# Kernel optimization log

Hardware: AMD Instinct MI355X
Metric: run time of the kernel (lower is better)

Reference implementation:

```python
import jax, jax.numpy as jnp
import numpy as np

EPS = 1e-8  # matches torch F.cosine_similarity eps default


def setup_inputs() -> dict:
    key = jax.random.key(0)
    k1, k2 = jax.random.split(key)
    z = jax.random.normal(k1, (8192, 256), dtype=jnp.float32)            # [N, d] node latents
    embedding_weight = jax.random.normal(k2, (4096, 256), dtype=jnp.float32)  # [V, d] codebook
    return {"z": z, "embedding_weight": embedding_weight}


def _l2_normalize(x):
    # torch cosine_similarity clamps each norm at eps before dividing
    n = jnp.sqrt(jnp.sum(x * x, axis=-1, keepdims=True))
    return x / jnp.maximum(n, EPS)


def reference(z, embedding_weight):
    # decode_edges: sigmoid(z @ z^T) -> [N, N]
    adj = jax.nn.sigmoid(jnp.matmul(z, z.T))

    # decode_node_features: cosine similarity of every node latent vs every
    # codebook vector, then argmax over the codebook axis. Instead of the
    # naive [N, V, d] broadcast, normalize both sides and take a single
    # [N, d] x [d, V] matmul -> [N, V], then reduce with argmax.
    zn = _l2_normalize(z)                   # [N, d]
    en = _l2_normalize(embedding_weight)    # [V, d]
    cosine_sim = jnp.matmul(zn, en.T)       # [N, V]
    decoded_indices = jnp.argmax(cosine_sim, axis=1)  # [N] int

    return adj, decoded_indices
```

## Files before the change

kernel.cpp:

```cpp
#include <hip/hip_runtime.h>
#include <stdint.h>

#define D_DIM 256
#define NZ 8192
#define NV 4096

typedef __bf16 bf16;
typedef __attribute__((ext_vector_type(8))) __bf16 bf16x8;
typedef __attribute__((ext_vector_type(4))) float f32x4;

__device__ __forceinline__ void stage16(const bf16* g, bf16* lbase, int lane) {
#if __has_builtin(__builtin_amdgcn_global_load_lds)
  __builtin_amdgcn_global_load_lds(
      (const __attribute__((address_space(1))) void*)(uintptr_t)g,
      (__attribute__((address_space(3))) void*)(uint32_t)(uintptr_t)lbase,
      16, 0, 0);
#else
  *(bf16x8*)(lbase + lane * 8) = *(const bf16x8*)g;
#endif
}

__global__ void split_kernel(const float* __restrict__ src, bf16* __restrict__ hi,
                             bf16* __restrict__ lo, int n) {
  const int stride = gridDim.x * blockDim.x;
  for (int i = blockIdx.x * blockDim.x + threadIdx.x; i < n; i += stride) {
    const float x = src[i];
    const bf16 h = (bf16)x;
    hi[i] = h;
    lo[i] = (bf16)(x - (float)h);
  }
}

__global__ void rownorm_kernel(const float* __restrict__ src, float* __restrict__ rinv,
                               unsigned long long* __restrict__ slots) {
  __shared__ float red[4];
  const int row = blockIdx.x;
  const int t = threadIdx.x;
  const float v = src[(size_t)row * D_DIM + t];
  float s = v * v;
#pragma unroll
  for (int off = 32; off; off >>= 1) s += __shfl_xor(s, off);
  if ((t & 63) == 0) red[t >> 6] = s;
  __syncthreads();
  if (t == 0) {
    const float tot = red[0] + red[1] + red[2] + red[3];
    rinv[row] = 1.0f / fmaxf(sqrtf(tot), 1e-8f);
    if (slots) slots[row] = 0ull;
  }
}

__device__ __forceinline__ unsigned long long packvc(float v, int col) {
  const uint32_t b = __float_as_uint(v);
  const uint32_t key = b ^ ((uint32_t)((int32_t)b >> 31) | 0x80000000u);
  return ((unsigned long long)key << 32) | (uint32_t)(~(uint32_t)col);
}

template <int MODE>
__global__ __launch_bounds__(256, 2) void gemm_kernel(
    const bf16* __restrict__ Ah, const bf16* __restrict__ Al,
    const bf16* __restrict__ Bh, const bf16* __restrict__ Bl, int N,
    float* __restrict__ out, const float* __restrict__ rinv_row,
    const float* __restrict__ rinv_col, unsigned long long* __restrict__ slots) {
  __shared__ bf16 lAh[128 * 32], lAl[128 * 32], lBh[128 * 32], lBl[128 * 32];
  const int tid = threadIdx.x;
  const int lane = tid & 63;
  const int w = tid >> 6;
  const int wr = w >> 1, wc = w & 1;
  const int l15 = lane & 15, q = lane >> 4;
  const int bm = blockIdx.y * 128;
  const int bn = blockIdx.x * 128;

  f32x4 acc[4][4] = {};

  for (int kt = 0; kt < 8; ++kt) {
    const int ko = kt * 32;
#pragma unroll
    for (int i = 0; i < 2; ++i) {
      const int c = w * 128 + i * 64 + lane;
      const int r = c >> 2;
      const int kb = (c & 3) << 3;
      const size_t ga = (size_t)(bm + r) * D_DIM + ko + kb;
      const size_t gb = (size_t)(bn + r) * D_DIM + ko + kb;
      const int lofs = (w * 128 + i * 64) * 8;
      stage16(Ah + ga, lAh + lofs, lane);
      stage16(Al + ga, lAl + lofs, lane);
      stage16(Bh + gb, lBh + lofs, lane);
      stage16(Bl + gb, lBl + lofs, lane);
    }
    __syncthreads();
    bf16x8 fah[4], fal[4], fbh[4], fbl[4];
#pragma unroll
    for (int ms = 0; ms < 4; ++ms) {
      const int m = wr * 64 + ms * 16 + l15;
      fah[ms] = *(const bf16x8*)&lAh[m * 32 + q * 8];
      fal[ms] = *(const bf16x8*)&lAl[m * 32 + q * 8];
    }
#pragma unroll
    for (int ns = 0; ns < 4; ++ns) {
      const int n = wc * 64 + ns * 16 + l15;
      fbh[ns] = *(const bf16x8*)&lBh[n * 32 + q * 8];
      fbl[ns] = *(const bf16x8*)&lBl[n * 32 + q * 8];
    }
#pragma unroll
    for (int ms = 0; ms < 4; ++ms)
#pragma unroll
      for (int ns = 0; ns < 4; ++ns) {
        acc[ms][ns] = __builtin_amdgcn_mfma_f32_16x16x32_bf16(fah[ms], fbh[ns], acc[ms][ns], 0, 0, 0);
        acc[ms][ns] = __builtin_amdgcn_mfma_f32_16x16x32_bf16(fah[ms], fbl[ns], acc[ms][ns], 0, 0, 0);
        acc[ms][ns] = __builtin_amdgcn_mfma_f32_16x16x32_bf16(fal[ms], fbh[ns], acc[ms][ns], 0, 0, 0);
      }
    __syncthreads();
  }

  if (MODE == 0) {
#pragma unroll
    for (int ms = 0; ms < 4; ++ms) {
      const int rb = bm + wr * 64 + ms * 16 + q * 4;
#pragma unroll
      for (int r = 0; r < 4; ++r) {
        const size_t ro = (size_t)(rb + r) * N;
#pragma unroll
        for (int ns = 0; ns < 4; ++ns) {
          const int col = bn + wc * 64 + ns * 16 + l15;
          const float v = acc[ms][ns][r];
          out[ro + col] = 1.0f / (1.0f + __expf(-v));
        }
      }
    }
  } else {
    float rc[4];
    int cols[4];
#pragma unroll
    for (int ns = 0; ns < 4; ++ns) {
      cols[ns] = bn + wc * 64 + ns * 16 + l15;
      rc[ns] = rinv_col[cols[ns]];
    }
#pragma unroll
    for (int ms = 0; ms < 4; ++ms) {
      const int rb = bm + wr * 64 + ms * 16 + q * 4;
#pragma unroll
      for (int r = 0; r < 4; ++r) {
        const int rowg = rb + r;
        const float rr = rinv_row[rowg];
        const size_t ro = (size_t)rowg * N;
        unsigned long long best = 0ull;
#pragma unroll
        for (int ns = 0; ns < 4; ++ns) {
          const float v = acc[ms][ns][r] * rc[ns] * rr;
          out[ro + cols[ns]] = v;
          const unsigned long long p = packvc(v, cols[ns]);
          best = p > best ? p : best;
        }
#pragma unroll
        for (int off = 1; off < 16; off <<= 1) {
          const unsigned long long o = __shfl_xor(best, off);
          best = o > best ? o : best;
        }
        if (l15 == 0) atomicMax(&slots[rowg], best);
      }
    }
  }
}

__device__ __forceinline__ double block_reduce(double v, double* red, int t) {
#pragma unroll
  for (int off = 32; off; off >>= 1) v += __shfl_xor(v, off);
  __syncthreads();
  if ((t & 63) == 0) red[t >> 6] = v;
  __syncthreads();
  return red[0] + red[1] + red[2] + red[3];
}

__global__ __launch_bounds__(256) void refine_kernel(
    const float* __restrict__ Dm, const unsigned long long* __restrict__ slots,
    const float* __restrict__ z, const float* __restrict__ E,
    float* __restrict__ out_idx) {
  __shared__ int s_cand[128];
  __shared__ int s_cnt;
  __shared__ double s_red[4];
  const int row = blockIdx.x;
  const int t = threadIdx.x;
  if (t == 0) s_cnt = 0;
  __syncthreads();

  const unsigned long long packed = slots[row];
  const uint32_t key = (uint32_t)(packed >> 32);
  const uint32_t fb = (key & 0x80000000u) ? (key ^ 0x80000000u) : ~key;
  const float M = __uint_as_float(fb);
  const float thr = M - 1e-3f;

  const f32x4* drow4 = (const f32x4*)(Dm + (size_t)row * NV);
  for (int c4 = t; c4 < NV / 4; c4 += 256) {
    const f32x4 v = drow4[c4];
#pragma unroll
    for (int j = 0; j < 4; ++j) {
      if (v[j] >= thr) {
        const int k = atomicAdd(&s_cnt, 1);
        if (k < 128) s_cand[k] = c4 * 4 + j;
      }
    }
  }
  __syncthreads();
  const int cnt = s_cnt < 128 ? s_cnt : 128;

  const double zv = (double)z[(size_t)row * D_DIM + t];
  const double sz2 = block_reduce(zv * zv, s_red, t);

  double v1 = -1e30, v2 = -1e30;
  int c1 = 0x7fffffff, c2 = 0x7fffffff;
  for (int i = 0; i < cnt; ++i) {
    const int c = s_cand[i];
    const double ev = (double)E[(size_t)c * D_DIM + t];
    const double dot = block_reduce(zv * ev, s_red, t);
    const double se2 = block_reduce(ev * ev, s_red, t);
    if (t == 0) {
      const double cv = dot / (fmax(sqrt(sz2), 1e-8) * fmax(sqrt(se2), 1e-8));
      if (cv > v1 || (cv == v1 && c < c1)) {
        v2 = v1; c2 = c1; v1 = cv; c1 = c;
      } else if (cv > v2 || (cv == v2 && c < c2)) {
        v2 = cv; c2 = c;
      }
    }
  }
  if (t == 0) {
    int pick = c1;
    if (c2 != 0x7fffffff && (v1 - v2) < 3e-7) pick = c2;
    out_idx[row] = (float)pick;
  }
}

extern "C" void kernel_launch(void* const* d_in, const int* in_sizes, int n_in,
                              void* d_out, int out_size, void* d_ws, size_t ws_size,
                              hipStream_t stream) {
  const float* z = (const float*)d_in[0];
  const float* E = (const float*)d_in[1];
  float* out = (float*)d_out;

  char* ws = (char*)d_ws;
  bf16* zh = (bf16*)ws;
  bf16* zl = zh + (size_t)NZ * D_DIM;
  bf16* eh = zl + (size_t)NZ * D_DIM;
  bf16* el = eh + (size_t)NV * D_DIM;
  float* rinvZ = (float*)(el + (size_t)NV * D_DIM);
  float* rinvE = rinvZ + NZ;
  unsigned long long* slots = (unsigned long long*)(rinvE + NV);

  float* Dm = out;
  float* idx_out = out + (size_t)NZ * NZ;

  split_kernel<<<2048, 256, 0, stream>>>(z, zh, zl, NZ * D_DIM);
  split_kernel<<<1024, 256, 0, stream>>>(E, eh, el, NV * D_DIM);
  rownorm_kernel<<<NZ, 256, 0, stream>>>(z, rinvZ, slots);
  rownorm_kernel<<<NV, 256, 0, stream>>>(E, rinvE, nullptr);

  dim3 g2(NV / 128, NZ / 128);
  gemm_kernel<1><<<g2, 256, 0, stream>>>(zh, zl, eh, el, NV, Dm, rinvZ, rinvE, slots);

  refine_kernel<<<NZ, 256, 0, stream>>>(Dm, slots, z, E, idx_out);

  dim3 g1(NZ / 128, NZ / 128);
  gemm_kernel<0><<<g1, 256, 0, stream>>>(zh, zl, zh, zl, NZ, out, nullptr, nullptr, nullptr);
}
```

Baseline: 458.3 us.

## Exploit adjacency symmetry, bf16-only cosine GEMM, fuse prep kernels

The adjacency GEMM now computes only upper-triangular 128x128 tiles (2080 blocks) and writes each off-diagonal tile twice, once transposed, roughly halving its MFMA work. The cosine GEMM uses only the hi bf16 parts, so it needs one MFMA per step instead of three. Its scratch matrix is stored as bf16, and the refine candidate threshold is widened to absorb the extra error. The split and rownorm kernels are merged into one prep kernel. The transposed stores are strided column writes, and the lower-precision candidate filter relies on the fp64 refine pass to stay exact.

```diff
diff --git a/kernel.cpp b/kernel.cpp
--- a/kernel.cpp
+++ b/kernel.cpp
@@ -1,5 +1,6 @@
 #include <hip/hip_runtime.h>
 #include <stdint.h>
+#include <math.h>
 
 #define D_DIM 256
 #define NZ 8192
@@ -9,43 +10,48 @@
 typedef __attribute__((ext_vector_type(8))) __bf16 bf16x8;
 typedef __attribute__((ext_vector_type(4))) float f32x4;
 
-__device__ __forceinline__ void stage16(const bf16* g, bf16* lbase, int lane) {
+__device__ __forceinline__ void stage16(const bf16* g, bf16* lbase) {
 #if __has_builtin(__builtin_amdgcn_global_load_lds)
   __builtin_amdgcn_global_load_lds(
       (const __attribute__((address_space(1))) void*)(uintptr_t)g,
       (__attribute__((address_space(3))) void*)(uint32_t)(uintptr_t)lbase,
       16, 0, 0);
-#else
-  *(bf16x8*)(lbase + lane * 8) = *(const bf16x8*)g;
 #endif
 }
 
-__global__ void split_kernel(const float* __restrict__ src, bf16* __restrict__ hi,
-                             bf16* __restrict__ lo, int n) {
-  const int stride = gridDim.x * blockDim.x;
-  for (int i = blockIdx.x * blockDim.x + threadIdx.x; i < n; i += stride) {
-    const float x = src[i];
-    const bf16 h = (bf16)x;
-    hi[i] = h;
-    lo[i] = (bf16)(x - (float)h);
-  }
-}
-
-__global__ void rownorm_kernel(const float* __restrict__ src, float* __restrict__ rinv,
-                               unsigned long long* __restrict__ slots) {
+__global__ void prep_kernel(const float* __restrict__ z, const float* __restrict__ E,
+                            bf16* __restrict__ zh, bf16* __restrict__ zl,
+                            bf16* __restrict__ eh, float* __restrict__ rinvZ,
+                            float* __restrict__ rinvE,
+                            unsigned long long* __restrict__ slots) {
   __shared__ float red[4];
   const int row = blockIdx.x;
   const int t = threadIdx.x;
-  const float v = src[(size_t)row * D_DIM + t];
-  float s = v * v;
+  const bool isZ = row < NZ;
+  const int r = isZ ? row : row - NZ;
+  const float* src = isZ ? z : E;
+  const float x = src[(size_t)r * D_DIM + t];
+  const bf16 h = (bf16)x;
+  if (isZ) {
+    zh[(size_t)r * D_DIM + t] = h;
+    zl[(size_t)r * D_DIM + t] = (bf16)(x - (float)h);
+  } else {
+    eh[(size_t)r * D_DIM + t] = h;
+  }
+  float s = x * x;
 #pragma unroll
   for (int off = 32; off; off >>= 1) s += __shfl_xor(s, off);
   if ((t & 63) == 0) red[t >> 6] = s;
   __syncthreads();
   if (t == 0) {
     const float tot = red[0] + red[1] + red[2] + red[3];
-    rinv[row] = 1.0f / fmaxf(sqrtf(tot), 1e-8f);
-    if (slots) slots[row] = 0ull;
+    const float rv = 1.0f / fmaxf(sqrtf(tot), 1e-8f);
+    if (isZ) {
+      rinvZ[r] = rv;
+      slots[r] = 0ull;
+    } else {
+      rinvE[r] = rv;
+    }
   }
 }
 
@@ -55,13 +61,11 @@
   return ((unsigned long long)key << 32) | (uint32_t)(~(uint32_t)col);
 }
 
-template <int MODE>
-__global__ __launch_bounds__(256, 2) void gemm_kernel(
-    const bf16* __restrict__ Ah, const bf16* __restrict__ Al,
-    const bf16* __restrict__ Bh, const bf16* __restrict__ Bl, int N,
-    float* __restrict__ out, const float* __restrict__ rinv_row,
-    const float* __restrict__ rinv_col, unsigned long long* __restrict__ slots) {
-  __shared__ bf16 lAh[128 * 32], lAl[128 * 32], lBh[128 * 32], lBl[128 * 32];
+__global__ __launch_bounds__(256, 2) void cos_kernel(
+    const bf16* __restrict__ Ah, const bf16* __restrict__ Bh, bf16* __restrict__ Dm,
+    const float* __restrict__ rinvZ, const float* __restrict__ rinvE,
+    unsigned long long* __restrict__ slots) {
+  __shared__ bf16 lAh[128 * 32], lBh[128 * 32];
   const int tid = threadIdx.x;
   const int lane = tid & 63;
   const int w = tid >> 6;
@@ -79,13 +83,96 @@
       const int c = w * 128 + i * 64 + lane;
       const int r = c >> 2;
       const int kb = (c & 3) << 3;
+      const int lofs = (w * 128 + i * 64) * 8;
+      stage16(Ah + (size_t)(bm + r) * D_DIM + ko + kb, lAh + lofs);
+      stage16(Bh + (size_t)(bn + r) * D_DIM + ko + kb, lBh + lofs);
+    }
+    __syncthreads();
+    bf16x8 fa[4], fb[4];
+#pragma unroll
+    for (int ms = 0; ms < 4; ++ms)
+      fa[ms] = *(const bf16x8*)&lAh[(wr * 64 + ms * 16 + l15) * 32 + q * 8];
+#pragma unroll
+    for (int ns = 0; ns < 4; ++ns)
+      fb[ns] = *(const bf16x8*)&lBh[(wc * 64 + ns * 16 + l15) * 32 + q * 8];
+#pragma unroll
+    for (int ms = 0; ms < 4; ++ms)
+#pragma unroll
+      for (int ns = 0; ns < 4; ++ns)
+        acc[ms][ns] = __builtin_amdgcn_mfma_f32_16x16x32_bf16(fa[ms], fb[ns], acc[ms][ns], 0, 0, 0);
+    __syncthreads();
+  }
+
+  float rc[4];
+  int cols[4];
+#pragma unroll
+  for (int ns = 0; ns < 4; ++ns) {
+    cols[ns] = bn + wc * 64 + ns * 16 + l15;
+    rc[ns] = rinvE[cols[ns]];
+  }
+#pragma unroll
+  for (int ms = 0; ms < 4; ++ms) {
+    const int rb = bm + wr * 64 + ms * 16 + q * 4;
+#pragma unroll
+    for (int r = 0; r < 4; ++r) {
+      const int rowg = rb + r;
+      const float rr = rinvZ[rowg];
+      bf16* drow = Dm + (size_t)rowg * NV;
+      unsigned long long best = 0ull;
+#pragma unroll
+      for (int ns = 0; ns < 4; ++ns) {
+        const float v = acc[ms][ns][r] * rc[ns] * rr;
+        drow[cols[ns]] = (bf16)v;
+        const unsigned long long p = packvc(v, cols[ns]);
+        best = p > best ? p : best;
+      }
+#pragma unroll
+      for (int off = 1; off < 16; off <<= 1) {
+        const unsigned long long o = __shfl_xor(best, off);
+        best = o > best ? o : best;
+      }
+      if (l15 == 0) atomicMax(&slots[rowg], best);
+    }
+  }
+}
+
+__device__ __forceinline__ int tri_base(int i) { return i * 64 - ((i * (i - 1)) >> 1); }
+
+__global__ __launch_bounds__(256, 2) void adj_kernel(const bf16* __restrict__ Ah,
+                                                     const bf16* __restrict__ Al,
+                                                     float* __restrict__ out) {
+  __shared__ bf16 lAh[128 * 32], lAl[128 * 32], lBh[128 * 32], lBl[128 * 32];
+  int k = blockIdx.x;
+  k = (k & 7) * 260 + (k >> 3);
+  const double disc = 4160.25 - 2.0 * (double)k;
+  int bi = (int)(64.5 - sqrt(disc));
+  while (tri_base(bi + 1) <= k) ++bi;
+  while (tri_base(bi) > k) --bi;
+  const int bj = bi + (k - tri_base(bi));
+  const int bm = bi * 128, bn = bj * 128;
+
+  const int tid = threadIdx.x;
+  const int lane = tid & 63;
+  const int w = tid >> 6;
+  const int wr = w >> 1, wc = w & 1;
+  const int l15 = lane & 15, q = lane >> 4;
+
+  f32x4 acc[4][4] = {};
+
+  for (int kt = 0; kt < 8; ++kt) {
+    const int ko = kt * 32;
+#pragma unroll
+    for (int i = 0; i < 2; ++i) {
+      const int c = w * 128 + i * 64 + lane;
+      const int r = c >> 2;
+      const int kb = (c & 3) << 3;
       const size_t ga = (size_t)(bm + r) * D_DIM + ko + kb;
       const size_t gb = (size_t)(bn + r) * D_DIM + ko + kb;
       const int lofs = (w * 128 + i * 64) * 8;
-      stage16(Ah + ga, lAh + lofs, lane);
-      stage16(Al + ga, lAl + lofs, lane);
-      stage16(Bh + gb, lBh + lofs, lane);
-      stage16(Bl + gb, lBl + lofs, lane);
+      stage16(Ah + ga, lAh + lofs);
+      stage16(Al + ga, lAl + lofs);
+      stage16(Ah + gb, lBh + lofs);
+      stage16(Al + gb, lBl + lofs);
     }
     __syncthreads();
     bf16x8 fah[4], fal[4], fbh[4], fbl[4];
@@ -112,51 +199,35 @@
     __syncthreads();
   }
 
-  if (MODE == 0) {
+#pragma unroll
+  for (int ms = 0; ms < 4; ++ms)
+#pragma unroll
+    for (int ns = 0; ns < 4; ++ns)
+#pragma unroll
+      for (int r = 0; r < 4; ++r)
+        acc[ms][ns][r] = __builtin_amdgcn_rcpf(1.0f + __expf(-acc[ms][ns][r]));
+
+#pragma unroll
+  for (int ms = 0; ms < 4; ++ms) {
+    const int rb = bm + wr * 64 + ms * 16 + q * 4;
+#pragma unroll
+    for (int r = 0; r < 4; ++r) {
+      const size_t ro = (size_t)(rb + r) * NZ;
+#pragma unroll
+      for (int ns = 0; ns < 4; ++ns) {
+        const int col = bn + wc * 64 + ns * 16 + l15;
+        out[ro + col] = acc[ms][ns][r];
+      }
+    }
+  }
+  if (bi != bj) {
 #pragma unroll
     for (int ms = 0; ms < 4; ++ms) {
       const int rb = bm + wr * 64 + ms * 16 + q * 4;
 #pragma unroll
-      for (int r = 0; r < 4; ++r) {
-        const size_t ro = (size_t)(rb + r) * N;
-#pragma unroll
-        for (int ns = 0; ns < 4; ++ns) {
-          const int col = bn + wc * 64 + ns * 16 + l15;
-          const float v = acc[ms][ns][r];
-          out[ro + col] = 1.0f / (1.0f + __expf(-v));
-        }
-      }
-    }
-  } else {
-    float rc[4];
-    int cols[4];
-#pragma unroll
-    for (int ns = 0; ns < 4; ++ns) {
-      cols[ns] = bn + wc * 64 + ns * 16 + l15;
-      rc[ns] = rinv_col[cols[ns]];
-    }
-#pragma unroll
-    for (int ms = 0; ms < 4; ++ms) {
-      const int rb = bm + wr * 64 + ms * 16 + q * 4;
-#pragma unroll
-      for (int r = 0; r < 4; ++r) {
-        const int rowg = rb + r;
-        const float rr = rinv_row[rowg];
-        const size_t ro = (size_t)rowg * N;
-        unsigned long long best = 0ull;
-#pragma unroll
-        for (int ns = 0; ns < 4; ++ns) {
-          const float v = acc[ms][ns][r] * rc[ns] * rr;
-          out[ro + cols[ns]] = v;
-          const unsigned long long p = packvc(v, cols[ns]);
-          best = p > best ? p : best;
-        }
-#pragma unroll
-        for (int off = 1; off < 16; off <<= 1) {
-          const unsigned long long o = __shfl_xor(best, off);
-          best = o > best ? o : best;
-        }
-        if (l15 == 0) atomicMax(&slots[rowg], best);
+      for (int ns = 0; ns < 4; ++ns) {
+        const int col = bn + wc * 64 + ns * 16 + l15;
+        *(f32x4*)&out[(size_t)col * NZ + rb] = acc[ms][ns];
       }
     }
   }
@@ -172,7 +243,7 @@
 }
 
 __global__ __launch_bounds__(256) void refine_kernel(
-    const float* __restrict__ Dm, const unsigned long long* __restrict__ slots,
+    const bf16* __restrict__ Dm, const unsigned long long* __restrict__ slots,
     const float* __restrict__ z, const float* __restrict__ E,
     float* __restrict__ out_idx) {
   __shared__ int s_cand[128];
@@ -187,16 +258,16 @@
   const uint32_t key = (uint32_t)(packed >> 32);
   const uint32_t fb = (key & 0x80000000u) ? (key ^ 0x80000000u) : ~key;
   const float M = __uint_as_float(fb);
-  const float thr = M - 1e-3f;
-
-  const f32x4* drow4 = (const f32x4*)(Dm + (size_t)row * NV);
-  for (int c4 = t; c4 < NV / 4; c4 += 256) {
-    const f32x4 v = drow4[c4];
-#pragma unroll
-    for (int j = 0; j < 4; ++j) {
-      if (v[j] >= thr) {
-        const int k = atomicAdd(&s_cnt, 1);
-        if (k < 128) s_cand[k] = c4 * 4 + j;
+  const float thr = M - 2e-2f;
+
+  const bf16* drow = Dm + (size_t)row * NV;
+  for (int c8 = t; c8 < NV / 8; c8 += 256) {
+    const bf16x8 v = *(const bf16x8*)(drow + c8 * 8);
+#pragma unroll
+    for (int j = 0; j < 8; ++j) {
+      if ((float)v[j] >= thr) {
+        const int kk = atomicAdd(&s_cnt, 1);
+        if (kk < 128) s_cand[kk] = c8 * 8 + j;
       }
     }
   }
@@ -240,24 +311,19 @@
   bf16* zh = (bf16*)ws;
   bf16* zl = zh + (size_t)NZ * D_DIM;
   bf16* eh = zl + (size_t)NZ * D_DIM;
-  bf16* el = eh + (size_t)NV * D_DIM;
-  float* rinvZ = (float*)(el + (size_t)NV * D_DIM);
+  float* rinvZ = (float*)(eh + (size_t)NV * D_DIM);
   float* rinvE = rinvZ + NZ;
   unsigned long long* slots = (unsigned long long*)(rinvE + NV);
 
-  float* Dm = out;
+  bf16* Dm = (bf16*)out;
   float* idx_out = out + (size_t)NZ * NZ;
 
-  split_kernel<<<2048, 256, 0, stream>>>(z, zh, zl, NZ * D_DIM);
-  split_kernel<<<1024, 256, 0, stream>>>(E, eh, el, NV * D_DIM);
-  rownorm_kernel<<<NZ, 256, 0, stream>>>(z, rinvZ, slots);
-  rownorm_kernel<<<NV, 256, 0, stream>>>(E, rinvE, nullptr);
+  prep_kernel<<<NZ + NV, 256, 0, stream>>>(z, E, zh, zl, eh, rinvZ, rinvE, slots);
 
   dim3 g2(NV / 128, NZ / 128);
-  gemm_kernel<1><<<g2, 256, 0, stream>>>(zh, zl, eh, el, NV, Dm, rinvZ, rinvE, slots);
+  cos_kernel<<<g2, 256, 0, stream>>>(zh, eh, Dm, rinvZ, rinvE, slots);
 
   refine_kernel<<<NZ, 256, 0, stream>>>(Dm, slots, z, E, idx_out);
 
-  dim3 g1(NZ / 128, NZ / 128);
-  gemm_kernel<0><<<g1, 256, 0, stream>>>(zh, zl, zh, zl, NZ, out, nullptr, nullptr, nullptr);
-}
+  adj_kernel<<<2080, 256, 0, stream>>>(zh, zl, out);
+}
```

After: 434.2 us. -5.3%, faster.
